# Performance work log

Measured on AMD Instinct MI355X. Metric: run time of the kernel, lower is better.

The kernel has to match this reference:

```python
import jax, jax.numpy as jnp
import numpy as np

H = 1024
L = 2

def setup_inputs() -> dict:
    key = jax.random.key(0)
    k1, k2, k3, k4, k5 = jax.random.split(key, 5)
    B, S = 32, 2048
    scale = 1.0 / np.sqrt(H)
    return {
        "query": jax.random.normal(k1, (B, 1, H * L), dtype=jnp.float32),
        "keys": jax.random.normal(k2, (B, S, H), dtype=jnp.float32),
        "Wa_w": jax.random.normal(k3, (H * L, H), dtype=jnp.float32) * scale,
        "Wa_b": jnp.zeros((H,), dtype=jnp.float32),
        "Ua_w": jax.random.normal(k4, (H, H), dtype=jnp.float32) * scale,
        "Ua_b": jnp.zeros((H,), dtype=jnp.float32),
        "Va_w": jax.random.normal(k5, (H, 1), dtype=jnp.float32) * scale,
        "Va_b": jnp.zeros((1,), dtype=jnp.float32),
    }

def reference(query, keys, Wa_w, Wa_b, Ua_w, Ua_b, Va_w, Va_b):
    # query: [B,1,H*L], keys: [B,S,H]
    q = jnp.einsum('bqd,dh->bqh', query, Wa_w) + Wa_b   # [B,1,H]
    k = jnp.einsum('bsd,dh->bsh', keys, Ua_w) + Ua_b    # [B,S,H]
    e = jnp.tanh(q + k)                                  # [B,S,H]
    scores = jnp.einsum('bsh,ho->bso', e, Va_w) + Va_b   # [B,S,1]
    scores = scores[:, :, 0][:, None, :]                 # [B,1,S]
    weights = jax.nn.softmax(scores, axis=-1)            # [B,1,S]
    context = jnp.einsum('bqs,bsh->bqh', weights, keys)  # [B,1,H]
    return (context, weights)
```

## Files before the change

### kernel.cpp

```cpp
#include <hip/hip_runtime.h>
#include <hip/hip_bf16.h>


typedef __attribute__((ext_vector_type(8))) short short8;
typedef __attribute__((ext_vector_type(4))) float floatx4;

typedef const __attribute__((address_space(1))) unsigned int gu32;
typedef __attribute__((address_space(3))) unsigned int lu32;

__device__ __forceinline__ unsigned short f2bf(float f) {
    union { float f; unsigned int u; } c; c.f = f;
    unsigned int u = c.u + 0x7fffu + ((c.u >> 16) & 1u);
    return (unsigned short)(u >> 16);
}

__device__ __forceinline__ unsigned int f2bf2(float lo, float hi) {
#if __has_builtin(__builtin_amdgcn_cvt_pk_bf16_f32)
    auto r = __builtin_amdgcn_cvt_pk_bf16_f32(lo, hi);
    unsigned int u; __builtin_memcpy(&u, &r, 4);
    return u;
#else
    return (unsigned int)f2bf(lo) | ((unsigned int)f2bf(hi) << 16);
#endif
}

__device__ __forceinline__ void gld16(const unsigned short* g, unsigned short* l) {
    __builtin_amdgcn_global_load_lds(
        (gu32*)(uintptr_t)g,
        (lu32*)(unsigned int)(uintptr_t)l,
        16, 0, 0);
}

__device__ __forceinline__ void kb16_chunk(const float* __restrict__ keys,
                                           unsigned short* __restrict__ kb,
                                           unsigned int t)
{
    unsigned int rg  = t >> 7;
    unsigned int rem = t & 127u;
    unsigned int g   = rem >> 2;
    unsigned int c   = rem & 3u;
    unsigned int p   = ((rg & 2047u) >> 1) & 3u;
    const float4* src = reinterpret_cast<const float4*>(keys + (size_t)rg*1024 + g*32 + c*8);
    float4 v0 = src[0], v1 = src[1];
    uint4 w;
    w.x = f2bf2(v0.x, v0.y); w.y = f2bf2(v0.z, v0.w);
    w.z = f2bf2(v1.x, v1.y); w.w = f2bf2(v1.z, v1.w);
    *reinterpret_cast<uint4*>(kb + (size_t)rg*1024 + g*32 + ((c ^ p) << 3)) = w;
}

__global__ __launch_bounds__(256) void pre_k(
    const float* __restrict__ query, const float* __restrict__ Wa,
    const float* __restrict__ Wab, const float* __restrict__ Uab,
    const float* __restrict__ Ua, const float* __restrict__ keys,
    float* __restrict__ qws, unsigned short* __restrict__ uat,
    unsigned short* __restrict__ kb, unsigned int kb_nch,
    float* __restrict__ score, float* __restrict__ out_ctx)
{
    __shared__ char smem[12288];
    const int tid = threadIdx.x;
    if (blockIdx.x < 512) {
        float* qs  = (float*)smem;
        float* red = (float*)(smem + 8192);
        const int b = blockIdx.x >> 4, hc = blockIdx.x & 15;
        #pragma unroll
        for (int i = 0; i < 8; i++) qs[tid + 256*i] = query[b*2048 + tid + 256*i];
        __syncthreads();
        const int hq = tid & 15;
        const int dg = tid >> 4;
        const float4* wp = reinterpret_cast<const float4*>(Wa + (size_t)(dg*128)*1024 + hc*64 + hq*4);
        const float* qp = qs + dg*128;
        float4 a0; a0.x = a0.y = a0.z = a0.w = 0.f;
        float4 a1; a1.x = a1.y = a1.z = a1.w = 0.f;
        #pragma unroll 4
        for (int d = 0; d < 128; d += 2) {
            float q0 = qp[d], q1 = qp[d+1];
            float4 w0 = wp[(size_t)d*256];
            float4 w1 = wp[(size_t)(d+1)*256];
            a0.x += q0*w0.x; a0.y += q0*w0.y; a0.z += q0*w0.z; a0.w += q0*w0.w;
            a1.x += q1*w1.x; a1.y += q1*w1.y; a1.z += q1*w1.z; a1.w += q1*w1.w;
        }
        a0.x += a1.x; a0.y += a1.y; a0.z += a1.z; a0.w += a1.w;
        *reinterpret_cast<float4*>(red + dg*64 + hq*4) = a0;
        __syncthreads();
        if (tid < 64) {
            float v = 0.f;
            #pragma unroll
            for (int g = 0; g < 16; g++) v += red[g*64 + tid];
            int hh = hc*64 + tid;
            qws[b*1024 + hh] = v + Wab[hh] + Uab[hh];
        }
    } else if (blockIdx.x < 768) {
        typedef unsigned short row_t[65];
        row_t* t = (row_t*)smem;
        const int q = blockIdx.x - 512;
        const int x = tid & 63, yy = tid >> 6;
        const int d0 = (q >> 4)*64, h0 = (q & 15)*64;
        #pragma unroll
        for (int i = 0; i < 16; i++) {
            int y = yy*16 + i;
            t[y][x] = f2bf(Ua[(size_t)(d0+y)*1024 + h0 + x]);
        }
        __syncthreads();
        #pragma unroll
        for (int i = 0; i < 16; i++) {
            int y = yy*16 + i;
            uat[(size_t)(h0+y)*1024 + d0 + x] = t[x][y];
        }
    } else if (blockIdx.x < 800) {
        float* p = score + (size_t)(blockIdx.x - 768) * 2048;
        for (int i = tid; i < 2048; i += 256) p[i] = 0.f;
    } else if (blockIdx.x < 832) {
        float* p = out_ctx + (size_t)(blockIdx.x - 800) * 1024;
        for (int i = tid; i < 1024; i += 256) p[i] = 0.f;
    } else {
        const unsigned int stride = (gridDim.x - 832u) * 256u;
        unsigned int t = (blockIdx.x - 832u)*256u + tid;
        #pragma unroll 4
        for (int it = 0; it < 4; ++it, t += stride)
            if (t < kb_nch) kb16_chunk(keys, kb, t);
    }
}

__global__ __launch_bounds__(256) void kb16_k(const float* __restrict__ keys,
                                              unsigned short* __restrict__ kb,
                                              unsigned int nch)
{
    const unsigned int stride = gridDim.x * 256u;
    unsigned int t = blockIdx.x * 256u + threadIdx.x;
    #pragma unroll 4
    for (int it = 0; it < 4; ++it, t += stride)
        if (t < nch) kb16_chunk(keys, kb, t);
}

__global__ __launch_bounds__(256) void score_gemm_fast(
    const unsigned short* __restrict__ kb16,
    const unsigned short* __restrict__ uat,
    const float* __restrict__ qws,
    const float* __restrict__ Va,
    float* __restrict__ score,
    int b0)
{
    __shared__ unsigned short aS[2][128*32];
    __shared__ unsigned short bS[2][256*32];
    const int tid = threadIdx.x;
    const int bz = blockIdx.z;
    const int b = b0 + bz;
    const int s0 = blockIdx.x * 128;
    const int h0 = blockIdx.y * 256;
    const int lane = tid & 63, wave = tid >> 6;
    const int quad = lane >> 4, l15 = lane & 15;
    const int wm = (wave & 1) * 64, wn = (wave >> 1) * 128;

    const int srow = lane >> 2;
    const int schunk = (lane & 3) ^ ((srow >> 1) & 3);
    const unsigned short* ubase = uat + (size_t)h0*1024;
    size_t boff[4];
    #pragma unroll
    for (int u = 0; u < 4; u++) {
        int cg = wave*4 + u;
        boff[u] = (size_t)(cg*16 + srow)*1024 + schunk*8;
    }

    const unsigned short* kA = kb16 + (size_t)(bz*2048 + s0)*1024;
    const size_t aoff0 = (size_t)(tid >> 2)*1024 + (size_t)(tid & 3)*8;
    const size_t aoff1 = (size_t)(64 + (tid >> 2))*1024 + (size_t)(tid & 3)*8;

    floatx4 acc[4][8];
    #pragma unroll
    for (int i = 0; i < 4; i++)
        #pragma unroll
        for (int j = 0; j < 8; j++) acc[i][j] = (floatx4)0.0f;

    gld16(kA + aoff0, aS[0] + wave*512);
    gld16(kA + aoff1, aS[0] + 2048 + wave*512);
    #pragma unroll
    for (int u = 0; u < 4; u++)
        gld16(ubase + boff[u], bS[0] + (wave*4 + u)*512);
    __syncthreads();

    int cur = 0;
    for (int kt = 0; kt < 31; ++kt) {
        const int nxt = cur ^ 1;
        const int k1 = (kt + 1) << 5;

        gld16(kA + aoff0 + k1, aS[nxt] + wave*512);
        gld16(kA + aoff1 + k1, aS[nxt] + 2048 + wave*512);
        #pragma unroll
        for (int u = 0; u < 4; u++)
            gld16(ubase + boff[u] + k1, bS[nxt] + (wave*4 + u)*512);

        short8 af[4], bf8[8];
        #pragma unroll
        for (int i = 0; i < 4; i++) {
            int row = wm + 16*i + l15;
            af[i] = *reinterpret_cast<const short8*>(aS[cur] + row*32 + ((quad ^ ((row>>1)&3)) * 8));
        }
        #pragma unroll
        for (int j = 0; j < 8; j++) {
            int row = wn + 16*j + l15;
            bf8[j] = *reinterpret_cast<const short8*>(bS[cur] + row*32 + ((quad ^ ((row>>1)&3)) * 8));
        }
        #pragma unroll
        for (int i = 0; i < 4; i++)
            #pragma unroll
            for (int j = 0; j < 8; j++)
                acc[i][j] = __builtin_amdgcn_mfma_f32_16x16x32_bf16(af[i], bf8[j], acc[i][j], 0, 0, 0);

        __syncthreads();
        cur = nxt;
    }

    {
        short8 af[4], bf8[8];
        #pragma unroll
        for (int i = 0; i < 4; i++) {
            int row = wm + 16*i + l15;
            af[i] = *reinterpret_cast<const short8*>(aS[cur] + row*32 + ((quad ^ ((row>>1)&3)) * 8));
        }
        #pragma unroll
        for (int j = 0; j < 8; j++) {
            int row = wn + 16*j + l15;
            bf8[j] = *reinterpret_cast<const short8*>(bS[cur] + row*32 + ((quad ^ ((row>>1)&3)) * 8));
        }
        #pragma unroll
        for (int i = 0; i < 4; i++)
            #pragma unroll
            for (int j = 0; j < 8; j++)
                acc[i][j] = __builtin_amdgcn_mfma_f32_16x16x32_bf16(af[i], bf8[j], acc[i][j], 0, 0, 0);
    }

    float qv[8], vav[8];
    #pragma unroll
    for (int j = 0; j < 8; j++) {
        int n = h0 + wn + 16*j + l15;
        qv[j]  = qws[b*1024 + n];
        vav[j] = Va[n];
    }
    #pragma unroll
    for (int i = 0; i < 4; i++) {
        #pragma unroll
        for (int r = 0; r < 4; r++) {
            float p = 0.f;
            #pragma unroll
            for (int j = 0; j < 8; j++) {
                float x = qv[j] + acc[i][j][r];
                float e = __expf(2.f * x);
                float t = 1.f - 2.f * __builtin_amdgcn_rcpf(e + 1.f);
                p += vav[j] * t;
            }
            #pragma unroll
            for (int off = 1; off < 16; off <<= 1) p += __shfl_xor(p, off, 64);
            if (l15 == 0) {
                int m = wm + 16*i + quad*4 + r;
                atomicAdd(score + (size_t)b*2048 + s0 + m, p);
            }
        }
    }
}

__global__ __launch_bounds__(256) void ctxsm_k(const float* __restrict__ keys,
                                               const float* __restrict__ score,
                                               float* __restrict__ out_w,
                                               float* __restrict__ out_ctx)
{
    const int tid = threadIdx.x;
    const int b = blockIdx.x, sc = blockIdx.y;
    __shared__ float wred[4], wred2[4], wv[32];
    float sv[8];
    float mx = -3.0e38f;
    #pragma unroll
    for (int i = 0; i < 8; i++) {
        sv[i] = score[(size_t)b*2048 + tid + 256*i];
        mx = fmaxf(mx, sv[i]);
    }
    #pragma unroll
    for (int off = 32; off >= 1; off >>= 1) mx = fmaxf(mx, __shfl_xor(mx, off, 64));
    if ((tid & 63) == 0) wred[tid >> 6] = mx;
    __syncthreads();
    mx = fmaxf(fmaxf(wred[0], wred[1]), fmaxf(wred[2], wred[3]));
    float lsum = 0.f;
    #pragma unroll
    for (int i = 0; i < 8; i++) lsum += __expf(sv[i] - mx);
    #pragma unroll
    for (int off = 32; off >= 1; off >>= 1) lsum += __shfl_xor(lsum, off, 64);
    if ((tid & 63) == 0) wred2[tid >> 6] = lsum;
    __syncthreads();
    const float inv = 1.0f / (wred2[0] + wred2[1] + wred2[2] + wred2[3]);
    if (tid < 32) {
        float e = __expf(score[(size_t)b*2048 + sc*32 + tid] - mx) * inv;
        wv[tid] = e;
        out_w[b*2048 + sc*32 + tid] = e;
    }
    __syncthreads();

    const float4* k4 = reinterpret_cast<const float4*>(keys) + (size_t)(b*2048 + sc*32)*256 + tid;
    float4 a; a.x = a.y = a.z = a.w = 0.f;
    #pragma unroll 4
    for (int s = 0; s < 32; s++) {
        float w = wv[s];
        float4 kv = k4[(size_t)s*256];
        a.x += w*kv.x; a.y += w*kv.y; a.z += w*kv.z; a.w += w*kv.w;
    }
    float* o = out_ctx + (size_t)b*1024 + tid*4;
    atomicAdd(o + 0, a.x);
    atomicAdd(o + 1, a.y);
    atomicAdd(o + 2, a.z);
    atomicAdd(o + 3, a.w);
}

extern "C" void kernel_launch(void* const* d_in, const int* in_sizes, int n_in,
                              void* d_out, int out_size, void* d_ws, size_t ws_size,
                              hipStream_t stream)
{
    const float* query = (const float*)d_in[0];
    const float* keys  = (const float*)d_in[1];
    const float* Wa_w  = (const float*)d_in[2];
    const float* Wa_b  = (const float*)d_in[3];
    const float* Ua_w  = (const float*)d_in[4];
    const float* Ua_b  = (const float*)d_in[5];
    const float* Va_w  = (const float*)d_in[6];

    char* ws = (char*)d_ws;
    float*          qws   = (float*)(ws);
    unsigned short* uat   = (unsigned short*)(ws + 131072);
    float*          score = (float*)(ws + 131072 + 2097152);
    const size_t BASE = 131072 + 2097152 + 4194304 + 2097152;
    unsigned short* kb16 = (unsigned short*)(ws + BASE);

    size_t avail = (ws_size > BASE) ? (ws_size - BASE) : 0;
    int nb = 32;
    while (nb > 1 && (size_t)nb * 2048 * 1024 * 2 > avail) nb >>= 1;

    float* out_ctx = (float*)d_out;
    float* out_w   = out_ctx + 32*1024;

    if (nb == 32) {
        const unsigned int nch = 32u * 2048u * 128u;
        pre_k<<<dim3(832 + 8192), 256, 0, stream>>>(
            query, Wa_w, Wa_b, Ua_b, Ua_w, keys, qws, uat, kb16, nch,
            score, out_ctx);
        score_gemm_fast<<<dim3(16, 4, 32), 256, 0, stream>>>(kb16, uat, qws, Va_w, score, 0);
    } else {
        pre_k<<<dim3(832), 256, 0, stream>>>(
            query, Wa_w, Wa_b, Ua_b, Ua_w, keys, qws, uat, kb16, 0u,
            score, out_ctx);
        for (int b0 = 0; b0 < 32; b0 += nb) {
            unsigned int nch = (unsigned int)nb * 2048u * 128u;
            unsigned int nblk = (nch/4u + 255u) / 256u;
            kb16_k<<<dim3(nblk), 256, 0, stream>>>(keys + (size_t)b0*2048*1024, kb16, nch);
            score_gemm_fast<<<dim3(16, 4, nb), 256, 0, stream>>>(kb16, uat, qws, Va_w, score, b0);
        }
    }
    ctxsm_k<<<dim3(32, 64), 256, 0, stream>>>(keys, score, out_w, out_ctx);
}
```

Baseline: 617.4 us.

## Fuse fp32-to-bf16 key conversion into score GEMM A-tile loads

Drops the separate pass that converts keys to a bf16 workspace copy. The score GEMM now reads fp32 keys directly, converts them in registers and writes the swizzled bf16 tile to shared memory, with the loads issued before the MFMA block so they overlap compute. This removes a full write and re-read of a 128 MB intermediate. In exchange, each of the 4 h-blocks re-reads the fp32 keys (twice the bytes of bf16), and the register staging raises register pressure in the GEMM loop.

```diff
diff --git a/kernel.cpp b/kernel.cpp
--- a/kernel.cpp
+++ b/kernel.cpp
@@ -31,29 +31,11 @@
         16, 0, 0);
 }
 
-__device__ __forceinline__ void kb16_chunk(const float* __restrict__ keys,
-                                           unsigned short* __restrict__ kb,
-                                           unsigned int t)
-{
-    unsigned int rg  = t >> 7;
-    unsigned int rem = t & 127u;
-    unsigned int g   = rem >> 2;
-    unsigned int c   = rem & 3u;
-    unsigned int p   = ((rg & 2047u) >> 1) & 3u;
-    const float4* src = reinterpret_cast<const float4*>(keys + (size_t)rg*1024 + g*32 + c*8);
-    float4 v0 = src[0], v1 = src[1];
-    uint4 w;
-    w.x = f2bf2(v0.x, v0.y); w.y = f2bf2(v0.z, v0.w);
-    w.z = f2bf2(v1.x, v1.y); w.w = f2bf2(v1.z, v1.w);
-    *reinterpret_cast<uint4*>(kb + (size_t)rg*1024 + g*32 + ((c ^ p) << 3)) = w;
-}
-
 __global__ __launch_bounds__(256) void pre_k(
     const float* __restrict__ query, const float* __restrict__ Wa,
     const float* __restrict__ Wab, const float* __restrict__ Uab,
-    const float* __restrict__ Ua, const float* __restrict__ keys,
+    const float* __restrict__ Ua,
     float* __restrict__ qws, unsigned short* __restrict__ uat,
-    unsigned short* __restrict__ kb, unsigned int kb_nch,
     float* __restrict__ score, float* __restrict__ out_ctx)
 {
     __shared__ char smem[12288];
@@ -109,42 +91,23 @@
     } else if (blockIdx.x < 800) {
         float* p = score + (size_t)(blockIdx.x - 768) * 2048;
         for (int i = tid; i < 2048; i += 256) p[i] = 0.f;
-    } else if (blockIdx.x < 832) {
+    } else {
         float* p = out_ctx + (size_t)(blockIdx.x - 800) * 1024;
         for (int i = tid; i < 1024; i += 256) p[i] = 0.f;
-    } else {
-        const unsigned int stride = (gridDim.x - 832u) * 256u;
-        unsigned int t = (blockIdx.x - 832u)*256u + tid;
-        #pragma unroll 4
-        for (int it = 0; it < 4; ++it, t += stride)
-            if (t < kb_nch) kb16_chunk(keys, kb, t);
-    }
-}
-
-__global__ __launch_bounds__(256) void kb16_k(const float* __restrict__ keys,
-                                              unsigned short* __restrict__ kb,
-                                              unsigned int nch)
-{
-    const unsigned int stride = gridDim.x * 256u;
-    unsigned int t = blockIdx.x * 256u + threadIdx.x;
-    #pragma unroll 4
-    for (int it = 0; it < 4; ++it, t += stride)
-        if (t < nch) kb16_chunk(keys, kb, t);
+    }
 }
 
 __global__ __launch_bounds__(256) void score_gemm_fast(
-    const unsigned short* __restrict__ kb16,
+    const float* __restrict__ keys,
     const unsigned short* __restrict__ uat,
     const float* __restrict__ qws,
     const float* __restrict__ Va,
-    float* __restrict__ score,
-    int b0)
+    float* __restrict__ score)
 {
     __shared__ unsigned short aS[2][128*32];
     __shared__ unsigned short bS[2][256*32];
     const int tid = threadIdx.x;
-    const int bz = blockIdx.z;
-    const int b = b0 + bz;
+    const int b  = blockIdx.z;
     const int s0 = blockIdx.x * 128;
     const int h0 = blockIdx.y * 256;
     const int lane = tid & 63, wave = tid >> 6;
@@ -161,9 +124,8 @@
         boff[u] = (size_t)(cg*16 + srow)*1024 + schunk*8;
     }
 
-    const unsigned short* kA = kb16 + (size_t)(bz*2048 + s0)*1024;
-    const size_t aoff0 = (size_t)(tid >> 2)*1024 + (size_t)(tid & 3)*8;
-    const size_t aoff1 = (size_t)(64 + (tid >> 2))*1024 + (size_t)(tid & 3)*8;
+    const float* kA = keys + (size_t)(b*2048 + s0)*1024;
+    const int arow0 = tid >> 2, ac = tid & 3;
 
     floatx4 acc[4][8];
     #pragma unroll
@@ -171,11 +133,21 @@
         #pragma unroll
         for (int j = 0; j < 8; j++) acc[i][j] = (floatx4)0.0f;
 
-    gld16(kA + aoff0, aS[0] + wave*512);
-    gld16(kA + aoff1, aS[0] + 2048 + wave*512);
     #pragma unroll
     for (int u = 0; u < 4; u++)
         gld16(ubase + boff[u], bS[0] + (wave*4 + u)*512);
+    #pragma unroll
+    for (int i = 0; i < 2; i++) {
+        int row = arow0 + 64*i;
+        int sl  = ac ^ ((row >> 1) & 3);
+        const float* gp = kA + (size_t)row*1024 + ac*8;
+        float4 v0 = *reinterpret_cast<const float4*>(gp);
+        float4 v1 = *reinterpret_cast<const float4*>(gp + 4);
+        uint4 w;
+        w.x = f2bf2(v0.x, v0.y); w.y = f2bf2(v0.z, v0.w);
+        w.z = f2bf2(v1.x, v1.y); w.w = f2bf2(v1.z, v1.w);
+        *reinterpret_cast<uint4*>(aS[0] + row*32 + sl*8) = w;
+    }
     __syncthreads();
 
     int cur = 0;
@@ -183,11 +155,17 @@
         const int nxt = cur ^ 1;
         const int k1 = (kt + 1) << 5;
 
-        gld16(kA + aoff0 + k1, aS[nxt] + wave*512);
-        gld16(kA + aoff1 + k1, aS[nxt] + 2048 + wave*512);
         #pragma unroll
         for (int u = 0; u < 4; u++)
             gld16(ubase + boff[u] + k1, bS[nxt] + (wave*4 + u)*512);
+        float4 pa0[2], pa1[2];
+        #pragma unroll
+        for (int i = 0; i < 2; i++) {
+            int row = arow0 + 64*i;
+            const float* gp = kA + (size_t)row*1024 + k1 + ac*8;
+            pa0[i] = *reinterpret_cast<const float4*>(gp);
+            pa1[i] = *reinterpret_cast<const float4*>(gp + 4);
+        }
 
         short8 af[4], bf8[8];
         #pragma unroll
@@ -206,6 +184,15 @@
             for (int j = 0; j < 8; j++)
                 acc[i][j] = __builtin_amdgcn_mfma_f32_16x16x32_bf16(af[i], bf8[j], acc[i][j], 0, 0, 0);
 
+        #pragma unroll
+        for (int i = 0; i < 2; i++) {
+            int row = arow0 + 64*i;
+            int sl  = ac ^ ((row >> 1) & 3);
+            uint4 w;
+            w.x = f2bf2(pa0[i].x, pa0[i].y); w.y = f2bf2(pa0[i].z, pa0[i].w);
+            w.z = f2bf2(pa1[i].x, pa1[i].y); w.w = f2bf2(pa1[i].z, pa1[i].w);
+            *reinterpret_cast<uint4*>(aS[nxt] + row*32 + sl*8) = w;
+        }
         __syncthreads();
         cur = nxt;
     }
@@ -324,32 +311,12 @@
     float*          qws   = (float*)(ws);
     unsigned short* uat   = (unsigned short*)(ws + 131072);
     float*          score = (float*)(ws + 131072 + 2097152);
-    const size_t BASE = 131072 + 2097152 + 4194304 + 2097152;
-    unsigned short* kb16 = (unsigned short*)(ws + BASE);
-
-    size_t avail = (ws_size > BASE) ? (ws_size - BASE) : 0;
-    int nb = 32;
-    while (nb > 1 && (size_t)nb * 2048 * 1024 * 2 > avail) nb >>= 1;
 
     float* out_ctx = (float*)d_out;
     float* out_w   = out_ctx + 32*1024;
 
-    if (nb == 32) {
-        const unsigned int nch = 32u * 2048u * 128u;
-        pre_k<<<dim3(832 + 8192), 256, 0, stream>>>(
-            query, Wa_w, Wa_b, Ua_b, Ua_w, keys, qws, uat, kb16, nch,
-            score, out_ctx);
-        score_gemm_fast<<<dim3(16, 4, 32), 256, 0, stream>>>(kb16, uat, qws, Va_w, score, 0);
-    } else {
-        pre_k<<<dim3(832), 256, 0, stream>>>(
-            query, Wa_w, Wa_b, Ua_b, Ua_w, keys, qws, uat, kb16, 0u,
-            score, out_ctx);
-        for (int b0 = 0; b0 < 32; b0 += nb) {
-            unsigned int nch = (unsigned int)nb * 2048u * 128u;
-            unsigned int nblk = (nch/4u + 255u) / 256u;
-            kb16_k<<<dim3(nblk), 256, 0, stream>>>(keys + (size_t)b0*2048*1024, kb16, nch);
-            score_gemm_fast<<<dim3(16, 4, nb), 256, 0, stream>>>(kb16, uat, qws, Va_w, score, b0);
-        }
-    }
+    pre_k<<<dim3(832), 256, 0, stream>>>(query, Wa_w, Wa_b, Ua_b, Ua_w,
+                                         qws, uat, score, out_ctx);
+    score_gemm_fast<<<dim3(16, 4, 32), 256, 0, stream>>>(keys, uat, qws, Va_w, score);
     ctxsm_k<<<dim3(32, 64), 256, 0, stream>>>(keys, score, out_w, out_ctx);
 }
```

After: 607.0 us. Within noise of the previous version (-1.7%).
